# Kernel optimization log

Hardware: AMD Instinct MI355X
Metric: run time of the kernel (lower is better)

The kernel has to match this reference:

```python
import jax, jax.numpy as jnp
import numpy as np

B, LQ, LKV = 4, 512, 8192
Q_DIM, KV_DIM = 1024, 512
QK_CH, V_CH, N_HEADS = 256, 256, 8
EPS = 1e-5


def _layernorm(x, g, b):
    m = jnp.mean(x, axis=-1, keepdims=True)
    v = jnp.mean(jnp.square(x - m), axis=-1, keepdims=True)
    return (x - m) * jax.lax.rsqrt(v + EPS) * g + b


def setup_inputs() -> dict:
    key = jax.random.key(0)
    ks = jax.random.split(key, 8)
    hidden_states = jax.random.normal(ks[0], (B, LQ, Q_DIM), dtype=jnp.float32)
    inputs = jax.random.normal(ks[1], (B, LKV, KV_DIM), dtype=jnp.float32)
    # Linear weights stored as [in, out] for x @ W
    Wq = jax.random.normal(ks[2], (Q_DIM, QK_CH), dtype=jnp.float32) * (1.0 / np.sqrt(Q_DIM))
    Wk = jax.random.normal(ks[3], (KV_DIM, QK_CH), dtype=jnp.float32) * (1.0 / np.sqrt(KV_DIM))
    Wv = jax.random.normal(ks[4], (KV_DIM, V_CH), dtype=jnp.float32) * (1.0 / np.sqrt(KV_DIM))
    bq = jnp.zeros((QK_CH,), jnp.float32)
    bk = jax.random.normal(ks[5], (QK_CH,), dtype=jnp.float32) * 0.02
    bv = jax.random.normal(ks[6], (V_CH,), dtype=jnp.float32) * 0.02
    ln1_g = jnp.ones((Q_DIM,), jnp.float32)
    ln1_b = jnp.zeros((Q_DIM,), jnp.float32)
    ln2_g = jnp.ones((KV_DIM,), jnp.float32)
    ln2_b = jnp.zeros((KV_DIM,), jnp.float32)
    return dict(hidden_states=hidden_states, inputs=inputs,
                ln1_g=ln1_g, ln1_b=ln1_b, ln2_g=ln2_g, ln2_b=ln2_b,
                Wq=Wq, bq=bq, Wk=Wk, bk=bk, Wv=Wv, bv=bv)


def reference(hidden_states, inputs, ln1_g, ln1_b, ln2_g, ln2_b,
              Wq, bq, Wk, bk, Wv, bv):
    H = N_HEADS
    dqk = QK_CH // H
    dv = V_CH // H
    hs = _layernorm(hidden_states, ln1_g, ln1_b)          # [B,LQ,Q_DIM]
    inp = _layernorm(inputs, ln2_g, ln2_b)                # [B,LKV,KV_DIM]
    q = (hs @ Wq + bq).reshape(B, LQ, H, dqk)             # [B,LQ,H,dqk]
    k = (inp @ Wk + bk).reshape(B, LKV, H, dqk)           # [B,LKV,H,dqk]
    v = (inp @ Wv + bv).reshape(B, LKV, H, dv)            # [B,LKV,H,dv]
    scores = jnp.einsum('bqhd,bkhd->bhqk', q, k) / np.sqrt(dqk).astype(np.float32)
    probs = jax.nn.softmax(scores, axis=-1)               # [B,H,LQ,LKV] (materialized, as in torch)
    ctx = jnp.einsum('bhqk,bkhd->bqhd', probs, v)         # [B,LQ,H,dv]
    return ctx.reshape(B, LQ, H * dv)
```

## Files before the change

kernel.cpp:

```cpp
#include <hip/hip_runtime.h>
#include <hip/hip_bf16.h>
#include <math.h>

#define NB    4
#define LQ    512
#define LKV   8192
#define QDIM  1024
#define KVDIM 512
#define NH    8
#define EPS_LN 1e-5f
#define SMAX  12.0f

typedef __attribute__((ext_vector_type(8))) short bf16x8;
typedef __attribute__((ext_vector_type(4))) float f32x4;

static __device__ __forceinline__ ushort f2bf(float x) {
    unsigned int u = __builtin_bit_cast(unsigned int, x);
    u += 0x7FFFu + ((u >> 16) & 1u);
    return (ushort)(u >> 16);
}

#if __has_builtin(__builtin_amdgcn_cvt_pk_bf16_f32)
static __device__ __forceinline__ unsigned int pk_bf16(float a, float b) {
    auto r = __builtin_amdgcn_cvt_pk_bf16_f32(a, b);
    return __builtin_bit_cast(unsigned int, r);
}
#else
static __device__ __forceinline__ unsigned int pk_bf16(float a, float b) {
    return (unsigned int)f2bf(a) | ((unsigned int)f2bf(b) << 16);
}
#endif

#if __has_builtin(__builtin_amdgcn_exp2f)
#define EXP2F(x) __builtin_amdgcn_exp2f(x)
#else
#define EXP2F(x) exp2f(x)
#endif

static __device__ __forceinline__ void gld_lds16(const ushort* g, ushort* l) {
    __builtin_amdgcn_global_load_lds(
        (const __attribute__((address_space(1))) unsigned int*)g,
        (__attribute__((address_space(3))) unsigned int*)l, 16, 0, 0);
}

template<int K>
static __device__ __forceinline__ void ln_norm_row(
    const float* __restrict__ x, const float* __restrict__ g,
    const float* __restrict__ bta, ushort* __restrict__ y, int row, int lane)
{
    const float* xp = x + (size_t)row * K;
    constexpr int NV = K / 256;
    float4 v[NV];
    float s = 0.f;
#pragma unroll
    for (int i = 0; i < NV; ++i) {
        v[i] = *(const float4*)(xp + lane * 4 + i * 256);
        s += v[i].x + v[i].y + v[i].z + v[i].w;
    }
#pragma unroll
    for (int o = 1; o < 64; o <<= 1) s += __shfl_xor(s, o, 64);
    const float mu = s * (1.0f / K);
    float vs = 0.f;
#pragma unroll
    for (int i = 0; i < NV; ++i) {
        float dx = v[i].x - mu, dy = v[i].y - mu, dz = v[i].z - mu, dw = v[i].w - mu;
        vs += dx * dx + dy * dy + dz * dz + dw * dw;
    }
#pragma unroll
    for (int o = 1; o < 64; o <<= 1) vs += __shfl_xor(vs, o, 64);
    const float rs = rsqrtf(vs * (1.0f / K) + EPS_LN);
#pragma unroll
    for (int i = 0; i < NV; ++i) {
        const float4 gv = *(const float4*)(g   + lane * 4 + i * 256);
        const float4 bv = *(const float4*)(bta + lane * 4 + i * 256);
        uint2 o;
        o.x = pk_bf16((v[i].x - mu) * rs * gv.x + bv.x, (v[i].y - mu) * rs * gv.y + bv.y);
        o.y = pk_bf16((v[i].z - mu) * rs * gv.z + bv.z, (v[i].w - mu) * rs * gv.w + bv.w);
        *(uint2*)(y + (size_t)row * K + lane * 4 + i * 256) = o;
    }
}

static __device__ __forceinline__ void ln_stats_row(
    const float* __restrict__ x, float* __restrict__ mean, float* __restrict__ rstd,
    int row, int lane)
{
    const float* xp = x + (size_t)row * QDIM;
    float4 v[4];
    float s = 0.f;
#pragma unroll
    for (int i = 0; i < 4; ++i) {
        v[i] = *(const float4*)(xp + lane * 4 + i * 256);
        s += v[i].x + v[i].y + v[i].z + v[i].w;
    }
#pragma unroll
    for (int o = 1; o < 64; o <<= 1) s += __shfl_xor(s, o, 64);
    const float mu = s * (1.0f / QDIM);
    float vs = 0.f;
#pragma unroll
    for (int i = 0; i < 4; ++i) {
        float dx = v[i].x - mu, dy = v[i].y - mu, dz = v[i].z - mu, dw = v[i].w - mu;
        vs += dx * dx + dy * dy + dz * dz + dw * dw;
    }
#pragma unroll
    for (int o = 1; o < 64; o <<= 1) vs += __shfl_xor(vs, o, 64);
    if (lane == 0) {
        mean[row] = mu;
        rstd[row] = rsqrtf(vs * (1.0f / QDIM) + EPS_LN);
    }
}

static __device__ __forceinline__ void wt_transpose_body(
    const float* __restrict__ src, ushort* __restrict__ dst, int K,
    int kx, int ny, int t, ushort (*Ts)[72])
{
    const int k0 = kx * 64, n0 = ny * 64;
    const int nl = t & 63;
#pragma unroll
    for (int p = 0; p < 16; ++p) {
        const int kl = p * 4 + (t >> 6);
        Ts[nl][kl] = f2bf(src[(size_t)(k0 + kl) * 256 + n0 + nl]);
    }
    __syncthreads();
    const int ck = (t & 7) * 8;
#pragma unroll
    for (int p = 0; p < 2; ++p) {
        const int rn = p * 32 + (t >> 3);
        *(bf16x8*)(dst + (size_t)(n0 + rn) * K + k0 + ck) = *(const bf16x8*)&Ts[rn][ck];
    }
}

__global__ __launch_bounds__(256) void phaseA_kernel(
    const float* __restrict__ inputs, const float* __restrict__ ln2g,
    const float* __restrict__ ln2b,   ushort* __restrict__ Abf,
    const float* __restrict__ hidden, float* __restrict__ mean_h, float* __restrict__ rstd_h,
    const float* __restrict__ Wq, const float* __restrict__ Wk, const float* __restrict__ Wv,
    ushort* __restrict__ WtQ, ushort* __restrict__ WtKV)
{
    __shared__ ushort Ts[64][72];
    const int bid = blockIdx.x;
    const int t = threadIdx.x;
    const int lane = t & 63;
    if (bid < 8192) {
        ln_norm_row<KVDIM>(inputs, ln2g, ln2b, Abf, bid * 4 + (t >> 6), lane);
    } else if (bid < 8704) {
        ln_stats_row(hidden, mean_h, rstd_h, (bid - 8192) * 4 + (t >> 6), lane);
    } else if (bid < 8768) {
        const int p = bid - 8704;
        wt_transpose_body(Wq, WtQ, QDIM, p & 15, p >> 4, t, Ts);
    } else if (bid < 8800) {
        const int p = bid - 8768;
        wt_transpose_body(Wk, WtKV, KVDIM, p & 7, p >> 3, t, Ts);
    } else {
        const int p = bid - 8800;
        wt_transpose_body(Wv, WtKV + (size_t)256 * KVDIM, KVDIM, p & 7, p >> 3, t, Ts);
    }
}

__global__ __launch_bounds__(256) void phaseB_kernel(
    const ushort* __restrict__ Abf, const ushort* __restrict__ WtKV,
    const float* __restrict__ bk, const float* __restrict__ bv,
    ushort* __restrict__ kb, ushort* __restrict__ vt,
    const float* __restrict__ hidden, const float* __restrict__ mean_h,
    const float* __restrict__ rstd_h,
    const float* __restrict__ ln1g, const float* __restrict__ ln1b,
    const ushort* __restrict__ WtQ, const float* __restrict__ bq,
    ushort* __restrict__ qb, float oscale)
{
    __shared__ __align__(16) ushort SMEM[4 * 64 * 72];
    const int bid  = blockIdx.x;
    const int t    = threadIdx.x;
    const int lane = t & 63;
    const int w    = t >> 6;
    const int lq   = lane & 15;
    const int lg   = lane >> 4;
    const int wm   = w >> 1;
    const int wn   = w & 1;

    if (bid < 1024) {
        const int bm = (bid >> 2) * 128;
        const int bn = (bid & 3) * 128;
        ushort* As = SMEM;
        ushort* Bs = SMEM + 4096;

        const int srow = t >> 2;
        const int scol = ((t & 3) ^ ((t >> 3) & 3)) * 8;
        const ushort* gA = Abf  + (size_t)(bm + srow) * KVDIM + scol;
        const ushort* gB = WtKV + (size_t)(bn + srow) * KVDIM + scol;
        ushort* lA = As + t * 8;
        ushort* lB = Bs + t * 8;

        f32x4 acc[4][4] = {};
        for (int k0 = 0; k0 < KVDIM; k0 += 32) {
            gld_lds16(gA + k0,                       lA);
            gld_lds16(gA + (size_t)64 * KVDIM + k0,  lA + 2048);
            gld_lds16(gB + k0,                       lB);
            gld_lds16(gB + (size_t)64 * KVDIM + k0,  lB + 2048);
            __syncthreads();
            bf16x8 af[4], bf[4];
#pragma unroll
            for (int mt = 0; mt < 4; ++mt) {
                const int m = wm * 64 + mt * 16 + lq;
                af[mt] = *(const bf16x8*)(As + m * 32 + ((lg ^ ((m >> 1) & 3)) << 3));
            }
#pragma unroll
            for (int nt = 0; nt < 4; ++nt) {
                const int n = wn * 64 + nt * 16 + lq;
                bf[nt] = *(const bf16x8*)(Bs + n * 32 + ((lg ^ ((n >> 1) & 3)) << 3));
            }
#pragma unroll
            for (int mt = 0; mt < 4; ++mt)
#pragma unroll
                for (int nt = 0; nt < 4; ++nt)
                    acc[mt][nt] = __builtin_amdgcn_mfma_f32_16x16x32_bf16(af[mt], bf[nt], acc[mt][nt], 0, 0, 0);
            __syncthreads();
        }
        const int m0base = bm + wm * 64;
        const int bidx   = m0base >> 13;
        const int tokb   = m0base & 8191;

        if (bn < 256) {
            ushort (*Cs)[72] = (ushort(*)[72])(SMEM + w * 64 * 72);
#pragma unroll
            for (int nt = 0; nt < 4; ++nt) {
                const int n_l = nt * 16 + lq;
                const float bias = bk[bn + wn * 64 + n_l];
#pragma unroll
                for (int mt = 0; mt < 4; ++mt)
#pragma unroll
                    for (int r = 0; r < 4; ++r)
                        Cs[mt * 16 + lg * 4 + r][n_l] = f2bf(acc[mt][nt][r] + bias);
            }
            const int r0 = lane >> 3;
            const int ck = (lane & 7) * 8;
            const int nc = bn + wn * 64 + ck;
            const int h = nc >> 5, d = nc & 31;
            const size_t obase = (((size_t)(bidx * NH + h) << 13) + tokb) * 32 + d;
#pragma unroll
            for (int p = 0; p < 8; ++p) {
                const int row = p * 8 + r0;
                *(bf16x8*)(kb + obase + (size_t)row * 32) = *(const bf16x8*)&Cs[row][ck];
            }
        } else {
            ushort (*Cs)[72] = (ushort(*)[72])(SMEM + w * 64 * 72);
#pragma unroll
            for (int nt = 0; nt < 4; ++nt) {
                const int n_l = nt * 16 + lq;
                const float bias = bv[(bn - 256) + wn * 64 + n_l];
#pragma unroll
                for (int mt = 0; mt < 4; ++mt) {
                    uint2 o;
                    o.x = pk_bf16(acc[mt][nt][0] + bias, acc[mt][nt][1] + bias);
                    o.y = pk_bf16(acc[mt][nt][2] + bias, acc[mt][nt][3] + bias);
                    *(uint2*)&Cs[n_l][mt * 16 + lg * 4] = o;
                }
            }
            const int r0 = lane >> 3;
            const int cm = (lane & 7) * 8;
            const int tokc = tokb + cm;
#pragma unroll
            for (int p = 0; p < 8; ++p) {
                const int row = p * 8 + r0;
                const int nv  = (bn - 256) + wn * 64 + row;
                const int h = nv >> 5, d = nv & 31;
                *(bf16x8*)(vt + ((size_t)(bidx * NH + h) * 32 + d) * LKV + tokc) =
                    *(const bf16x8*)&Cs[row][cm];
            }
        }
    } else {
        const int p  = bid - 1024;
        const int bm = (p >> 2) * 64;
        const int bn = (p & 3) * 64;
        ushort* As = SMEM;
        ushort* Bs = SMEM + 4096;

        const int srow = t >> 3;
        const int scol = ((t & 7) ^ (srow & 7)) * 8;
        const ushort* gB = WtQ + (size_t)(bn + srow) * QDIM + scol;
        ushort* lB  = Bs + t * 8;
        ushort* lA0 = As + t * 8;
        ushort* lA1 = As + 2048 + t * 8;

        const int r0 = bm + srow;
        const float mu0 = mean_h[r0],      rs0 = rstd_h[r0];
        const float mu1 = mean_h[r0 + 32], rs1 = rstd_h[r0 + 32];
        const float* xA0 = hidden + (size_t)r0 * QDIM + scol;
        const float* xA1 = xA0 + (size_t)32 * QDIM;

        f32x4 acc[2][2] = {};
        for (int k0 = 0; k0 < QDIM; k0 += 64) {
            gld_lds16(gB + k0,                      lB);
            gld_lds16(gB + (size_t)32 * QDIM + k0,  lB + 2048);
            const float4 a0 = *(const float4*)(xA0 + k0);
            const float4 a1 = *(const float4*)(xA0 + k0 + 4);
            const float4 c0 = *(const float4*)(xA1 + k0);
            const float4 c1 = *(const float4*)(xA1 + k0 + 4);
            const float4 g0 = *(const float4*)(ln1g + k0 + scol);
            const float4 g1 = *(const float4*)(ln1g + k0 + scol + 4);
            const float4 d0 = *(const float4*)(ln1b + k0 + scol);
            const float4 d1 = *(const float4*)(ln1b + k0 + scol + 4);
            uint4 w0, w1;
            w0.x = pk_bf16((a0.x - mu0) * rs0 * g0.x + d0.x, (a0.y - mu0) * rs0 * g0.y + d0.y);
            w0.y = pk_bf16((a0.z - mu0) * rs0 * g0.z + d0.z, (a0.w - mu0) * rs0 * g0.w + d0.w);
            w0.z = pk_bf16((a1.x - mu0) * rs0 * g1.x + d1.x, (a1.y - mu0) * rs0 * g1.y + d1.y);
            w0.w = pk_bf16((a1.z - mu0) * rs0 * g1.z + d1.z, (a1.w - mu0) * rs0 * g1.w + d1.w);
            w1.x = pk_bf16((c0.x - mu1) * rs1 * g0.x + d0.x, (c0.y - mu1) * rs1 * g0.y + d0.y);
            w1.y = pk_bf16((c0.z - mu1) * rs1 * g0.z + d0.z, (c0.w - mu1) * rs1 * g0.w + d0.w);
            w1.z = pk_bf16((c1.x - mu1) * rs1 * g1.x + d1.x, (c1.y - mu1) * rs1 * g1.y + d1.y);
            w1.w = pk_bf16((c1.z - mu1) * rs1 * g1.z + d1.z, (c1.w - mu1) * rs1 * g1.w + d1.w);
            *(uint4*)lA0 = w0;
            *(uint4*)lA1 = w1;
            __syncthreads();
#pragma unroll
            for (int kh = 0; kh < 2; ++kh) {
                bf16x8 af[2], bf[2];
#pragma unroll
                for (int mt = 0; mt < 2; ++mt) {
                    const int m = wm * 32 + mt * 16 + lq;
                    af[mt] = *(const bf16x8*)(As + m * 64 + (((lg + 4 * kh) ^ (m & 7)) << 3));
                }
#pragma unroll
                for (int nt = 0; nt < 2; ++nt) {
                    const int n = wn * 32 + nt * 16 + lq;
                    bf[nt] = *(const bf16x8*)(Bs + n * 64 + (((lg + 4 * kh) ^ (n & 7)) << 3));
                }
#pragma unroll
                for (int mt = 0; mt < 2; ++mt)
#pragma unroll
                    for (int nt = 0; nt < 2; ++nt)
                        acc[mt][nt] = __builtin_amdgcn_mfma_f32_16x16x32_bf16(af[mt], bf[nt], acc[mt][nt], 0, 0, 0);
            }
            __syncthreads();
        }

#pragma unroll
        for (int nt = 0; nt < 2; ++nt) {
            const int n = bn + wn * 32 + nt * 16 + lq;
            const int h = n >> 5, d = n & 31;
            const float bias = bq[n];
#pragma unroll
            for (int mt = 0; mt < 2; ++mt) {
                const int m0   = bm + wm * 32 + mt * 16 + lg * 4;
                const int bidx = m0 >> 9;
                const int tok  = m0 & 511;
                const size_t base = (((size_t)(bidx * NH + h) << 9) + tok) * 32 + d;
#pragma unroll
                for (int r = 0; r < 4; ++r)
                    qb[base + (size_t)r * 32] = f2bf((acc[mt][nt][r] + bias) * oscale);
            }
        }
    }
}

__global__ __launch_bounds__(512, 4) void attn_mfma_kernel(
    const ushort* __restrict__ Qb,
    const ushort* __restrict__ Kb,
    const ushort* __restrict__ Vt,
    float* __restrict__ Out)
{
    const int bid = blockIdx.x;
    const int xcd = bid & 7;
    const int rr  = bid >> 3;
    const int bh  = ((rr & 3) << 3) | xcd;
    const int qt  = rr >> 2;
    const int b = bh >> 3, h = bh & 7;
    const int t = threadIdx.x, w = t >> 6, lane = t & 63;
    const int lq = lane & 15, lg = lane >> 4;

    __shared__ __align__(16) ushort Pb[2][8][32][72];
    __shared__ float lbuf[8][32];

    bf16x8 qfrag[2];
    const size_t qbase = ((size_t)bh * LQ + qt * 32) * 32;
    qfrag[0] = *(const bf16x8*)(Qb + qbase + (size_t)lq * 32 + lg * 8);
    qfrag[1] = *(const bf16x8*)(Qb + qbase + (size_t)(16 + lq) * 32 + lg * 8);

    const ushort* KpA = Kb + ((size_t)bh * LKV + w * 1024 + lq) * 32 + lg * 8;
    const ushort* VpA = Vt + ((size_t)bh * 32 + lq) * LKV + w * 1024 + lg * 8;

    f32x4 oacc[2][2] = {};
    float l_part[2] = {0.f, 0.f};
    const f32x4 cM = {-SMAX, -SMAX, -SMAX, -SMAX};

    bf16x8 kf[4], vf[2][2];
#pragma unroll
    for (int m = 0; m < 4; ++m)
        kf[m] = *(const bf16x8*)(KpA + (size_t)(m * 16) * 32);
#pragma unroll
    for (int dt = 0; dt < 2; ++dt)
#pragma unroll
        for (int hf = 0; hf < 2; ++hf)
            vf[dt][hf] = *(const bf16x8*)(VpA + (size_t)(dt * 16) * LKV + hf * 32);

    for (int kt = 0; kt < 1024; kt += 64) {
        bf16x8 kc[4], vc[2][2];
#pragma unroll
        for (int m = 0; m < 4; ++m) kc[m] = kf[m];
#pragma unroll
        for (int dt = 0; dt < 2; ++dt)
#pragma unroll
            for (int hf = 0; hf < 2; ++hf) vc[dt][hf] = vf[dt][hf];

        const int nk = (kt + 64 < 1024) ? kt + 64 : 0;
#pragma unroll
        for (int m = 0; m < 4; ++m)
            kf[m] = *(const bf16x8*)(KpA + (size_t)(nk + m * 16) * 32);
#pragma unroll
        for (int dt = 0; dt < 2; ++dt)
#pragma unroll
            for (int hf = 0; hf < 2; ++hf)
                vf[dt][hf] = *(const bf16x8*)(VpA + (size_t)(dt * 16) * LKV + nk + hf * 32);

        f32x4 s[4][2];
#pragma unroll
        for (int m = 0; m < 4; ++m)
#pragma unroll
            for (int n = 0; n < 2; ++n)
                s[m][n] = __builtin_amdgcn_mfma_f32_16x16x32_bf16(kc[m], qfrag[n], cM, 0, 0, 0);

        ushort* myP = &Pb[(kt >> 6) & 1][w][0][0];

#pragma unroll
        for (int n = 0; n < 2; ++n) {
#pragma unroll
            for (int m = 0; m < 4; ++m) {
                const float p0 = EXP2F(s[m][n][0]);
                const float p1 = EXP2F(s[m][n][1]);
                const float p2 = EXP2F(s[m][n][2]);
                const float p3 = EXP2F(s[m][n][3]);
                l_part[n] += ((p0 + p1) + (p2 + p3));
                uint2 pw;
                pw.x = pk_bf16(p0, p1);
                pw.y = pk_bf16(p2, p3);
                *(uint2*)(myP + (n * 16 + lq) * 72 + m * 16 + lg * 4) = pw;
            }
        }

        bf16x8 pf[2][2];
#pragma unroll
        for (int n = 0; n < 2; ++n)
#pragma unroll
            for (int hf = 0; hf < 2; ++hf)
                pf[n][hf] = *(const bf16x8*)(myP + (size_t)(n * 16 + lq) * 72 + hf * 32 + lg * 8);

#pragma unroll
        for (int dt = 0; dt < 2; ++dt)
#pragma unroll
            for (int n = 0; n < 2; ++n) {
                oacc[dt][n] = __builtin_amdgcn_mfma_f32_16x16x32_bf16(vc[dt][0], pf[n][0], oacc[dt][n], 0, 0, 0);
                oacc[dt][n] = __builtin_amdgcn_mfma_f32_16x16x32_bf16(vc[dt][1], pf[n][1], oacc[dt][n], 0, 0, 0);
            }
    }

#pragma unroll
    for (int n = 0; n < 2; ++n) {
        l_part[n] += __shfl_xor(l_part[n], 16);
        l_part[n] += __shfl_xor(l_part[n], 32);
    }
    if (lg == 0) {
        lbuf[w][lq]      = l_part[0];
        lbuf[w][16 + lq] = l_part[1];
    }
    __syncthreads();

    float* Ob = (float*)&Pb[0][0][0][0];
    if (w >= 4) {
#pragma unroll
        for (int n = 0; n < 2; ++n)
#pragma unroll
            for (int dt = 0; dt < 2; ++dt)
                *(f32x4*)&Ob[((size_t)(w - 4) * 32 + n * 16 + lq) * 36 + dt * 16 + lg * 4] = oacc[dt][n];
    }
    __syncthreads();
    if (w < 4) {
#pragma unroll
        for (int n = 0; n < 2; ++n)
#pragma unroll
            for (int dt = 0; dt < 2; ++dt) {
                float* p = &Ob[((size_t)w * 32 + n * 16 + lq) * 36 + dt * 16 + lg * 4];
                f32x4 v = *(f32x4*)p;
                v += oacc[dt][n];
                *(f32x4*)p = v;
            }
    }
    __syncthreads();
    {
        const int q  = t >> 4;
        const int d0 = (t & 15) * 2;
        float s0 = 0.f, s1 = 0.f;
#pragma unroll
        for (int j = 0; j < 4; ++j) {
            s0 += Ob[((size_t)j * 32 + q) * 36 + d0];
            s1 += Ob[((size_t)j * 32 + q) * 36 + d0 + 1];
        }
        float gl = 0.f;
#pragma unroll
        for (int j = 0; j < 8; ++j) gl += lbuf[j][q];
        const float inv = 1.0f / gl;
        float2 o; o.x = s0 * inv; o.y = s1 * inv;
        *(float2*)(Out + ((size_t)b * LQ + qt * 32 + q) * 256 + h * 32 + d0) = o;
    }
}

extern "C" void kernel_launch(void* const* d_in, const int* in_sizes, int n_in,
                              void* d_out, int out_size, void* d_ws, size_t ws_size,
                              hipStream_t stream)
{
    const float* hidden = (const float*)d_in[0];
    const float* inputs = (const float*)d_in[1];
    const float* ln1g   = (const float*)d_in[2];
    const float* ln1b   = (const float*)d_in[3];
    const float* ln2g   = (const float*)d_in[4];
    const float* ln2b   = (const float*)d_in[5];
    const float* Wq     = (const float*)d_in[6];
    const float* bq     = (const float*)d_in[7];
    const float* Wk     = (const float*)d_in[8];
    const float* bk     = (const float*)d_in[9];
    const float* Wv     = (const float*)d_in[10];
    const float* bv     = (const float*)d_in[11];
    float* out = (float*)d_out;

    char* wsb = (char*)d_ws;
    ushort* qb     = (ushort*)(wsb);
    ushort* WtKV   = (ushort*)(wsb + (1u << 20));
    ushort* WtQ    = (ushort*)(wsb + (1u << 20) + (512u << 10));
    float*  mean_h = (float*)(wsb + (2u << 20));
    float*  rstd_h = (float*)(wsb + (2u << 20) + 8192);
    ushort* kb     = (ushort*)(wsb + (2u << 20) + 16384);
    ushort* vt     = (ushort*)(wsb + (18u << 20) + 16384);
    ushort* Abf    = (ushort*)(wsb + (34u << 20) + 16384);

    const float oscale = 0.2550540226496112f;

    phaseA_kernel<<<8832, 256, 0, stream>>>(inputs, ln2g, ln2b, Abf,
                                            hidden, mean_h, rstd_h,
                                            Wq, Wk, Wv, WtQ, WtKV);
    phaseB_kernel<<<1152, 256, 0, stream>>>(Abf, WtKV, bk, bv, kb, vt,
                                            hidden, mean_h, rstd_h, ln1g, ln1b,
                                            WtQ, bq, qb, oscale);
    attn_mfma_kernel<<<512, 512, 0, stream>>>(qb, kb, vt, out);
}
```

Measured before the change: 215.1 us.

## Fuse KV layernorm into projection GEMM, retile Q GEMM, software-pipeline attention loop

Phase A now computes only per-row mean and rstd for the KV inputs, using single-pass sum and sum-of-squares. The normalized bf16 copy of the inputs is no longer written; the KV projection GEMM normalizes fp32 inputs on the fly with a register prefetch of the next k-slice and an XCD-aware block remap. The Q GEMM uses smaller tiles (more blocks) with prefetched LN inputs. The attention inner loop is restructured into 32-key steps with a double-buffered P tile, overlapping the PV MFMAs of the previous step with the QK and exp of the current one. Single-pass variance is less numerically robust, and the KV GEMM now reads fp32 activations, four times per row (once per N tile).

```diff
diff --git a/kernel.cpp b/kernel.cpp
--- a/kernel.cpp
+++ b/kernel.cpp
@@ -43,72 +43,6 @@
         (__attribute__((address_space(3))) unsigned int*)l, 16, 0, 0);
 }
 
-template<int K>
-static __device__ __forceinline__ void ln_norm_row(
-    const float* __restrict__ x, const float* __restrict__ g,
-    const float* __restrict__ bta, ushort* __restrict__ y, int row, int lane)
-{
-    const float* xp = x + (size_t)row * K;
-    constexpr int NV = K / 256;
-    float4 v[NV];
-    float s = 0.f;
-#pragma unroll
-    for (int i = 0; i < NV; ++i) {
-        v[i] = *(const float4*)(xp + lane * 4 + i * 256);
-        s += v[i].x + v[i].y + v[i].z + v[i].w;
-    }
-#pragma unroll
-    for (int o = 1; o < 64; o <<= 1) s += __shfl_xor(s, o, 64);
-    const float mu = s * (1.0f / K);
-    float vs = 0.f;
-#pragma unroll
-    for (int i = 0; i < NV; ++i) {
-        float dx = v[i].x - mu, dy = v[i].y - mu, dz = v[i].z - mu, dw = v[i].w - mu;
-        vs += dx * dx + dy * dy + dz * dz + dw * dw;
-    }
-#pragma unroll
-    for (int o = 1; o < 64; o <<= 1) vs += __shfl_xor(vs, o, 64);
-    const float rs = rsqrtf(vs * (1.0f / K) + EPS_LN);
-#pragma unroll
-    for (int i = 0; i < NV; ++i) {
-        const float4 gv = *(const float4*)(g   + lane * 4 + i * 256);
-        const float4 bv = *(const float4*)(bta + lane * 4 + i * 256);
-        uint2 o;
-        o.x = pk_bf16((v[i].x - mu) * rs * gv.x + bv.x, (v[i].y - mu) * rs * gv.y + bv.y);
-        o.y = pk_bf16((v[i].z - mu) * rs * gv.z + bv.z, (v[i].w - mu) * rs * gv.w + bv.w);
-        *(uint2*)(y + (size_t)row * K + lane * 4 + i * 256) = o;
-    }
-}
-
-static __device__ __forceinline__ void ln_stats_row(
-    const float* __restrict__ x, float* __restrict__ mean, float* __restrict__ rstd,
-    int row, int lane)
-{
-    const float* xp = x + (size_t)row * QDIM;
-    float4 v[4];
-    float s = 0.f;
-#pragma unroll
-    for (int i = 0; i < 4; ++i) {
-        v[i] = *(const float4*)(xp + lane * 4 + i * 256);
-        s += v[i].x + v[i].y + v[i].z + v[i].w;
-    }
-#pragma unroll
-    for (int o = 1; o < 64; o <<= 1) s += __shfl_xor(s, o, 64);
-    const float mu = s * (1.0f / QDIM);
-    float vs = 0.f;
-#pragma unroll
-    for (int i = 0; i < 4; ++i) {
-        float dx = v[i].x - mu, dy = v[i].y - mu, dz = v[i].z - mu, dw = v[i].w - mu;
-        vs += dx * dx + dy * dy + dz * dz + dw * dw;
-    }
-#pragma unroll
-    for (int o = 1; o < 64; o <<= 1) vs += __shfl_xor(vs, o, 64);
-    if (lane == 0) {
-        mean[row] = mu;
-        rstd[row] = rsqrtf(vs * (1.0f / QDIM) + EPS_LN);
-    }
-}
-
 static __device__ __forceinline__ void wt_transpose_body(
     const float* __restrict__ src, ushort* __restrict__ dst, int K,
     int kx, int ny, int t, ushort (*Ts)[72])
@@ -130,8 +64,7 @@
 }
 
 __global__ __launch_bounds__(256) void phaseA_kernel(
-    const float* __restrict__ inputs, const float* __restrict__ ln2g,
-    const float* __restrict__ ln2b,   ushort* __restrict__ Abf,
+    const float* __restrict__ inputs, float* __restrict__ mean_i, float* __restrict__ rstd_i,
     const float* __restrict__ hidden, float* __restrict__ mean_h, float* __restrict__ rstd_h,
     const float* __restrict__ Wq, const float* __restrict__ Wk, const float* __restrict__ Wv,
     ushort* __restrict__ WtQ, ushort* __restrict__ WtKV)
@@ -141,9 +74,39 @@
     const int t = threadIdx.x;
     const int lane = t & 63;
     if (bid < 8192) {
-        ln_norm_row<KVDIM>(inputs, ln2g, ln2b, Abf, bid * 4 + (t >> 6), lane);
+        const int row = bid * 4 + (t >> 6);
+        const float* xp = inputs + (size_t)row * KVDIM;
+        float s = 0.f, ss = 0.f;
+#pragma unroll
+        for (int i = 0; i < 2; ++i) {
+            const float4 v = *(const float4*)(xp + lane * 4 + i * 256);
+            s  += (v.x + v.y) + (v.z + v.w);
+            ss += (v.x * v.x + v.y * v.y) + (v.z * v.z + v.w * v.w);
+        }
+#pragma unroll
+        for (int o = 1; o < 64; o <<= 1) { s += __shfl_xor(s, o, 64); ss += __shfl_xor(ss, o, 64); }
+        if (lane == 0) {
+            const float mu = s * (1.0f / KVDIM);
+            mean_i[row] = mu;
+            rstd_i[row] = rsqrtf(ss * (1.0f / KVDIM) - mu * mu + EPS_LN);
+        }
     } else if (bid < 8704) {
-        ln_stats_row(hidden, mean_h, rstd_h, (bid - 8192) * 4 + (t >> 6), lane);
+        const int row = (bid - 8192) * 4 + (t >> 6);
+        const float* xp = hidden + (size_t)row * QDIM;
+        float s = 0.f, ss = 0.f;
+#pragma unroll
+        for (int i = 0; i < 4; ++i) {
+            const float4 v = *(const float4*)(xp + lane * 4 + i * 256);
+            s  += (v.x + v.y) + (v.z + v.w);
+            ss += (v.x * v.x + v.y * v.y) + (v.z * v.z + v.w * v.w);
+        }
+#pragma unroll
+        for (int o = 1; o < 64; o <<= 1) { s += __shfl_xor(s, o, 64); ss += __shfl_xor(ss, o, 64); }
+        if (lane == 0) {
+            const float mu = s * (1.0f / QDIM);
+            mean_h[row] = mu;
+            rstd_h[row] = rsqrtf(ss * (1.0f / QDIM) - mu * mu + EPS_LN);
+        }
     } else if (bid < 8768) {
         const int p = bid - 8704;
         wt_transpose_body(Wq, WtQ, QDIM, p & 15, p >> 4, t, Ts);
@@ -157,11 +120,14 @@
 }
 
 __global__ __launch_bounds__(256) void phaseB_kernel(
-    const ushort* __restrict__ Abf, const ushort* __restrict__ WtKV,
+    const float* __restrict__ inputs,
+    const float* __restrict__ mean_i, const float* __restrict__ rstd_i,
+    const float* __restrict__ ln2g, const float* __restrict__ ln2b,
+    const ushort* __restrict__ WtKV,
     const float* __restrict__ bk, const float* __restrict__ bv,
     ushort* __restrict__ kb, ushort* __restrict__ vt,
-    const float* __restrict__ hidden, const float* __restrict__ mean_h,
-    const float* __restrict__ rstd_h,
+    const float* __restrict__ hidden,
+    const float* __restrict__ mean_h, const float* __restrict__ rstd_h,
     const float* __restrict__ ln1g, const float* __restrict__ ln1b,
     const ushort* __restrict__ WtQ, const float* __restrict__ bq,
     ushort* __restrict__ qb, float oscale)
@@ -177,24 +143,59 @@
     const int wn   = w & 1;
 
     if (bid < 1024) {
-        const int bm = (bid >> 2) * 128;
-        const int bn = (bid & 3) * 128;
+        const int x  = bid & 7;
+        const int j  = bid >> 3;
+        const int bm = (x * 32 + (j >> 2)) * 128;
+        const int bn = (j & 3) * 128;
         ushort* As = SMEM;
         ushort* Bs = SMEM + 4096;
 
         const int srow = t >> 2;
         const int scol = ((t & 3) ^ ((t >> 3) & 3)) * 8;
-        const ushort* gA = Abf  + (size_t)(bm + srow) * KVDIM + scol;
         const ushort* gB = WtKV + (size_t)(bn + srow) * KVDIM + scol;
-        ushort* lA = As + t * 8;
-        ushort* lB = Bs + t * 8;
+        ushort* lB  = Bs + t * 8;
+        ushort* lA0 = As + t * 8;
+        ushort* lA1 = As + 2048 + t * 8;
+
+        const int r0 = bm + srow;
+        const float rs0 = rstd_i[r0],      mr0 = -mean_i[r0] * rs0;
+        const float rs1 = rstd_i[r0 + 64], mr1 = -mean_i[r0 + 64] * rs1;
+        const float* xp0 = inputs + (size_t)r0 * KVDIM + scol;
+        const float* xp1 = xp0 + (size_t)64 * KVDIM;
+
+        float4 a0 = *(const float4*)(xp0);
+        float4 a1 = *(const float4*)(xp0 + 4);
+        float4 c0 = *(const float4*)(xp1);
+        float4 c1 = *(const float4*)(xp1 + 4);
+        float4 g0 = *(const float4*)(ln2g + scol);
+        float4 g1 = *(const float4*)(ln2g + scol + 4);
+        float4 e0 = *(const float4*)(ln2b + scol);
+        float4 e1 = *(const float4*)(ln2b + scol + 4);
 
         f32x4 acc[4][4] = {};
         for (int k0 = 0; k0 < KVDIM; k0 += 32) {
-            gld_lds16(gA + k0,                       lA);
-            gld_lds16(gA + (size_t)64 * KVDIM + k0,  lA + 2048);
             gld_lds16(gB + k0,                       lB);
             gld_lds16(gB + (size_t)64 * KVDIM + k0,  lB + 2048);
+            uint4 w0, w1;
+            w0.x = pk_bf16(fmaf(fmaf(a0.x, rs0, mr0), g0.x, e0.x), fmaf(fmaf(a0.y, rs0, mr0), g0.y, e0.y));
+            w0.y = pk_bf16(fmaf(fmaf(a0.z, rs0, mr0), g0.z, e0.z), fmaf(fmaf(a0.w, rs0, mr0), g0.w, e0.w));
+            w0.z = pk_bf16(fmaf(fmaf(a1.x, rs0, mr0), g1.x, e1.x), fmaf(fmaf(a1.y, rs0, mr0), g1.y, e1.y));
+            w0.w = pk_bf16(fmaf(fmaf(a1.z, rs0, mr0), g1.z, e1.z), fmaf(fmaf(a1.w, rs0, mr0), g1.w, e1.w));
+            w1.x = pk_bf16(fmaf(fmaf(c0.x, rs1, mr1), g0.x, e0.x), fmaf(fmaf(c0.y, rs1, mr1), g0.y, e0.y));
+            w1.y = pk_bf16(fmaf(fmaf(c0.z, rs1, mr1), g0.z, e0.z), fmaf(fmaf(c0.w, rs1, mr1), g0.w, e0.w));
+            w1.z = pk_bf16(fmaf(fmaf(c1.x, rs1, mr1), g1.x, e1.x), fmaf(fmaf(c1.y, rs1, mr1), g1.y, e1.y));
+            w1.w = pk_bf16(fmaf(fmaf(c1.z, rs1, mr1), g1.z, e1.z), fmaf(fmaf(c1.w, rs1, mr1), g1.w, e1.w));
+            *(uint4*)lA0 = w0;
+            *(uint4*)lA1 = w1;
+            const int nk = (k0 + 32 < KVDIM) ? k0 + 32 : 0;
+            a0 = *(const float4*)(xp0 + nk);
+            a1 = *(const float4*)(xp0 + nk + 4);
+            c0 = *(const float4*)(xp1 + nk);
+            c1 = *(const float4*)(xp1 + nk + 4);
+            g0 = *(const float4*)(ln2g + nk + scol);
+            g1 = *(const float4*)(ln2g + nk + scol + 4);
+            e0 = *(const float4*)(ln2b + nk + scol);
+            e1 = *(const float4*)(ln2b + nk + scol + 4);
             __syncthreads();
             bf16x8 af[4], bf[4];
 #pragma unroll
@@ -214,6 +215,7 @@
                     acc[mt][nt] = __builtin_amdgcn_mfma_f32_16x16x32_bf16(af[mt], bf[nt], acc[mt][nt], 0, 0, 0);
             __syncthreads();
         }
+
         const int m0base = bm + wm * 64;
         const int bidx   = m0base >> 13;
         const int tokb   = m0base & 8191;
@@ -230,14 +232,14 @@
                     for (int r = 0; r < 4; ++r)
                         Cs[mt * 16 + lg * 4 + r][n_l] = f2bf(acc[mt][nt][r] + bias);
             }
-            const int r0 = lane >> 3;
-            const int ck = (lane & 7) * 8;
-            const int nc = bn + wn * 64 + ck;
+            const int r0_ = lane >> 3;
+            const int ck  = (lane & 7) * 8;
+            const int nc  = bn + wn * 64 + ck;
             const int h = nc >> 5, d = nc & 31;
             const size_t obase = (((size_t)(bidx * NH + h) << 13) + tokb) * 32 + d;
 #pragma unroll
             for (int p = 0; p < 8; ++p) {
-                const int row = p * 8 + r0;
+                const int row = p * 8 + r0_;
                 *(bf16x8*)(kb + obase + (size_t)row * 32) = *(const bf16x8*)&Cs[row][ck];
             }
         } else {
@@ -254,12 +256,12 @@
                     *(uint2*)&Cs[n_l][mt * 16 + lg * 4] = o;
                 }
             }
-            const int r0 = lane >> 3;
-            const int cm = (lane & 7) * 8;
+            const int r0_ = lane >> 3;
+            const int cm  = (lane & 7) * 8;
             const int tokc = tokb + cm;
 #pragma unroll
             for (int p = 0; p < 8; ++p) {
-                const int row = p * 8 + r0;
+                const int row = p * 8 + r0_;
                 const int nv  = (bn - 256) + wn * 64 + row;
                 const int h = nv >> 5, d = nv & 31;
                 *(bf16x8*)(vt + ((size_t)(bidx * NH + h) * 32 + d) * LKV + tokc) =
@@ -268,66 +270,58 @@
         }
     } else {
         const int p  = bid - 1024;
-        const int bm = (p >> 2) * 64;
-        const int bn = (p & 3) * 64;
+        const int x  = p & 7;
+        const int j  = p >> 3;
+        const int bm = (x * 8 + (j >> 2)) * 32;
+        const int bn = (j & 3) * 64;
         ushort* As = SMEM;
-        ushort* Bs = SMEM + 4096;
+        ushort* Bs = SMEM + 2048;
 
         const int srow = t >> 3;
         const int scol = ((t & 7) ^ (srow & 7)) * 8;
         const ushort* gB = WtQ + (size_t)(bn + srow) * QDIM + scol;
-        ushort* lB  = Bs + t * 8;
-        ushort* lA0 = As + t * 8;
-        ushort* lA1 = As + 2048 + t * 8;
-
-        const int r0 = bm + srow;
-        const float mu0 = mean_h[r0],      rs0 = rstd_h[r0];
-        const float mu1 = mean_h[r0 + 32], rs1 = rstd_h[r0 + 32];
-        const float* xA0 = hidden + (size_t)r0 * QDIM + scol;
-        const float* xA1 = xA0 + (size_t)32 * QDIM;
-
-        f32x4 acc[2][2] = {};
+        ushort* lB = Bs + t * 8;
+        ushort* lA = As + t * 8;
+
+        const int r = bm + srow;
+        const float rs0 = rstd_h[r], mr0 = -mean_h[r] * rs0;
+        const float* xA = hidden + (size_t)r * QDIM + scol;
+
+        float4 a0 = *(const float4*)(xA);
+        float4 a1 = *(const float4*)(xA + 4);
+        float4 g0 = *(const float4*)(ln1g + scol);
+        float4 g1 = *(const float4*)(ln1g + scol + 4);
+        float4 e0 = *(const float4*)(ln1b + scol);
+        float4 e1 = *(const float4*)(ln1b + scol + 4);
+
+        f32x4 acc[2] = {};
         for (int k0 = 0; k0 < QDIM; k0 += 64) {
             gld_lds16(gB + k0,                      lB);
             gld_lds16(gB + (size_t)32 * QDIM + k0,  lB + 2048);
-            const float4 a0 = *(const float4*)(xA0 + k0);
-            const float4 a1 = *(const float4*)(xA0 + k0 + 4);
-            const float4 c0 = *(const float4*)(xA1 + k0);
-            const float4 c1 = *(const float4*)(xA1 + k0 + 4);
-            const float4 g0 = *(const float4*)(ln1g + k0 + scol);
-            const float4 g1 = *(const float4*)(ln1g + k0 + scol + 4);
-            const float4 d0 = *(const float4*)(ln1b + k0 + scol);
-            const float4 d1 = *(const float4*)(ln1b + k0 + scol + 4);
-            uint4 w0, w1;
-            w0.x = pk_bf16((a0.x - mu0) * rs0 * g0.x + d0.x, (a0.y - mu0) * rs0 * g0.y + d0.y);
-            w0.y = pk_bf16((a0.z - mu0) * rs0 * g0.z + d0.z, (a0.w - mu0) * rs0 * g0.w + d0.w);
-            w0.z = pk_bf16((a1.x - mu0) * rs0 * g1.x + d1.x, (a1.y - mu0) * rs0 * g1.y + d1.y);
-            w0.w = pk_bf16((a1.z - mu0) * rs0 * g1.z + d1.z, (a1.w - mu0) * rs0 * g1.w + d1.w);
-            w1.x = pk_bf16((c0.x - mu1) * rs1 * g0.x + d0.x, (c0.y - mu1) * rs1 * g0.y + d0.y);
-            w1.y = pk_bf16((c0.z - mu1) * rs1 * g0.z + d0.z, (c0.w - mu1) * rs1 * g0.w + d0.w);
-            w1.z = pk_bf16((c1.x - mu1) * rs1 * g1.x + d1.x, (c1.y - mu1) * rs1 * g1.y + d1.y);
-            w1.w = pk_bf16((c1.z - mu1) * rs1 * g1.z + d1.z, (c1.w - mu1) * rs1 * g1.w + d1.w);
-            *(uint4*)lA0 = w0;
-            *(uint4*)lA1 = w1;
+            uint4 w0;
+            w0.x = pk_bf16(fmaf(fmaf(a0.x, rs0, mr0), g0.x, e0.x), fmaf(fmaf(a0.y, rs0, mr0), g0.y, e0.y));
+            w0.y = pk_bf16(fmaf(fmaf(a0.z, rs0, mr0), g0.z, e0.z), fmaf(fmaf(a0.w, rs0, mr0), g0.w, e0.w));
+            w0.z = pk_bf16(fmaf(fmaf(a1.x, rs0, mr0), g1.x, e1.x), fmaf(fmaf(a1.y, rs0, mr0), g1.y, e1.y));
+            w0.w = pk_bf16(fmaf(fmaf(a1.z, rs0, mr0), g1.z, e1.z), fmaf(fmaf(a1.w, rs0, mr0), g1.w, e1.w));
+            *(uint4*)lA = w0;
+            const int nk = (k0 + 64 < QDIM) ? k0 + 64 : 0;
+            a0 = *(const float4*)(xA + nk);
+            a1 = *(const float4*)(xA + nk + 4);
+            g0 = *(const float4*)(ln1g + nk + scol);
+            g1 = *(const float4*)(ln1g + nk + scol + 4);
+            e0 = *(const float4*)(ln1b + nk + scol);
+            e1 = *(const float4*)(ln1b + nk + scol + 4);
             __syncthreads();
 #pragma unroll
             for (int kh = 0; kh < 2; ++kh) {
-                bf16x8 af[2], bf[2];
-#pragma unroll
-                for (int mt = 0; mt < 2; ++mt) {
-                    const int m = wm * 32 + mt * 16 + lq;
-                    af[mt] = *(const bf16x8*)(As + m * 64 + (((lg + 4 * kh) ^ (m & 7)) << 3));
-                }
+                const int m = wm * 16 + lq;
+                const bf16x8 af = *(const bf16x8*)(As + m * 64 + (((lg + 4 * kh) ^ (m & 7)) << 3));
 #pragma unroll
                 for (int nt = 0; nt < 2; ++nt) {
                     const int n = wn * 32 + nt * 16 + lq;
-                    bf[nt] = *(const bf16x8*)(Bs + n * 64 + (((lg + 4 * kh) ^ (n & 7)) << 3));
+                    const bf16x8 bf = *(const bf16x8*)(Bs + n * 64 + (((lg + 4 * kh) ^ (n & 7)) << 3));
+                    acc[nt] = __builtin_amdgcn_mfma_f32_16x16x32_bf16(af, bf, acc[nt], 0, 0, 0);
                 }
-#pragma unroll
-                for (int mt = 0; mt < 2; ++mt)
-#pragma unroll
-                    for (int nt = 0; nt < 2; ++nt)
-                        acc[mt][nt] = __builtin_amdgcn_mfma_f32_16x16x32_bf16(af[mt], bf[nt], acc[mt][nt], 0, 0, 0);
             }
             __syncthreads();
         }
@@ -337,16 +331,13 @@
             const int n = bn + wn * 32 + nt * 16 + lq;
             const int h = n >> 5, d = n & 31;
             const float bias = bq[n];
-#pragma unroll
-            for (int mt = 0; mt < 2; ++mt) {
-                const int m0   = bm + wm * 32 + mt * 16 + lg * 4;
-                const int bidx = m0 >> 9;
-                const int tok  = m0 & 511;
-                const size_t base = (((size_t)(bidx * NH + h) << 9) + tok) * 32 + d;
-#pragma unroll
-                for (int r = 0; r < 4; ++r)
-                    qb[base + (size_t)r * 32] = f2bf((acc[mt][nt][r] + bias) * oscale);
-            }
+            const int m0   = bm + wm * 16 + lg * 4;
+            const int bidx = m0 >> 9;
+            const int tok  = m0 & 511;
+            const size_t base = (((size_t)(bidx * NH + h) << 9) + tok) * 32 + d;
+#pragma unroll
+            for (int rr_ = 0; rr_ < 4; ++rr_)
+                qb[base + (size_t)rr_ * 32] = f2bf((acc[nt][rr_] + bias) * oscale);
         }
     }
 }
@@ -366,7 +357,7 @@
     const int t = threadIdx.x, w = t >> 6, lane = t & 63;
     const int lq = lane & 15, lg = lane >> 4;
 
-    __shared__ __align__(16) ushort Pb[2][8][32][72];
+    __shared__ __align__(16) ushort Pb[2][8][32][40];
     __shared__ float lbuf[8][32];
 
     bf16x8 qfrag[2];
@@ -381,75 +372,86 @@
     float l_part[2] = {0.f, 0.f};
     const f32x4 cM = {-SMAX, -SMAX, -SMAX, -SMAX};
 
-    bf16x8 kf[4], vf[2][2];
-#pragma unroll
-    for (int m = 0; m < 4; ++m)
-        kf[m] = *(const bf16x8*)(KpA + (size_t)(m * 16) * 32);
-#pragma unroll
-    for (int dt = 0; dt < 2; ++dt)
-#pragma unroll
-        for (int hf = 0; hf < 2; ++hf)
-            vf[dt][hf] = *(const bf16x8*)(VpA + (size_t)(dt * 16) * LKV + hf * 32);
-
-    for (int kt = 0; kt < 1024; kt += 64) {
-        bf16x8 kc[4], vc[2][2];
-#pragma unroll
-        for (int m = 0; m < 4; ++m) kc[m] = kf[m];
-#pragma unroll
-        for (int dt = 0; dt < 2; ++dt)
-#pragma unroll
-            for (int hf = 0; hf < 2; ++hf) vc[dt][hf] = vf[dt][hf];
-
-        const int nk = (kt + 64 < 1024) ? kt + 64 : 0;
-#pragma unroll
-        for (int m = 0; m < 4; ++m)
-            kf[m] = *(const bf16x8*)(KpA + (size_t)(nk + m * 16) * 32);
-#pragma unroll
-        for (int dt = 0; dt < 2; ++dt)
-#pragma unroll
-            for (int hf = 0; hf < 2; ++hf)
-                vf[dt][hf] = *(const bf16x8*)(VpA + (size_t)(dt * 16) * LKV + nk + hf * 32);
-
-        f32x4 s[4][2];
-#pragma unroll
-        for (int m = 0; m < 4; ++m)
-#pragma unroll
-            for (int n = 0; n < 2; ++n)
-                s[m][n] = __builtin_amdgcn_mfma_f32_16x16x32_bf16(kc[m], qfrag[n], cM, 0, 0, 0);
-
-        ushort* myP = &Pb[(kt >> 6) & 1][w][0][0];
-
-#pragma unroll
-        for (int n = 0; n < 2; ++n) {
-#pragma unroll
-            for (int m = 0; m < 4; ++m) {
-                const float p0 = EXP2F(s[m][n][0]);
-                const float p1 = EXP2F(s[m][n][1]);
-                const float p2 = EXP2F(s[m][n][2]);
-                const float p3 = EXP2F(s[m][n][3]);
-                l_part[n] += ((p0 + p1) + (p2 + p3));
-                uint2 pw;
-                pw.x = pk_bf16(p0, p1);
-                pw.y = pk_bf16(p2, p3);
-                *(uint2*)(myP + (n * 16 + lq) * 72 + m * 16 + lg * 4) = pw;
-            }
-        }
-
-        bf16x8 pf[2][2];
-#pragma unroll
-        for (int n = 0; n < 2; ++n)
-#pragma unroll
-            for (int hf = 0; hf < 2; ++hf)
-                pf[n][hf] = *(const bf16x8*)(myP + (size_t)(n * 16 + lq) * 72 + hf * 32 + lg * 8);
-
-#pragma unroll
-        for (int dt = 0; dt < 2; ++dt)
-#pragma unroll
-            for (int n = 0; n < 2; ++n) {
-                oacc[dt][n] = __builtin_amdgcn_mfma_f32_16x16x32_bf16(vc[dt][0], pf[n][0], oacc[dt][n], 0, 0, 0);
-                oacc[dt][n] = __builtin_amdgcn_mfma_f32_16x16x32_bf16(vc[dt][1], pf[n][1], oacc[dt][n], 0, 0, 0);
-            }
-    }
+    ushort* P0 = &Pb[0][w][0][0];
+    ushort* P1 = &Pb[1][w][0][0];
+
+    bf16x8 kf0 = *(const bf16x8*)(KpA);
+    bf16x8 kf1 = *(const bf16x8*)(KpA + 16 * 32);
+    bf16x8 vf0 = *(const bf16x8*)(VpA);
+    bf16x8 vf1 = *(const bf16x8*)(VpA + (size_t)16 * LKV);
+
+    bf16x8 vp0, vp1;
+
+#define ATTN_EXPW(Pdst, s00, s10, s01, s11)                                              \
+    do {                                                                                 \
+        float p0, p1, p2, p3; uint2 pw;                                                  \
+        p0 = EXP2F((s00)[0]); p1 = EXP2F((s00)[1]); p2 = EXP2F((s00)[2]); p3 = EXP2F((s00)[3]); \
+        l_part[0] += (p0 + p1) + (p2 + p3);                                              \
+        pw.x = pk_bf16(p0, p1); pw.y = pk_bf16(p2, p3);                                  \
+        *(uint2*)((Pdst) + (lq) * 40 + lg * 4) = pw;                                     \
+        p0 = EXP2F((s10)[0]); p1 = EXP2F((s10)[1]); p2 = EXP2F((s10)[2]); p3 = EXP2F((s10)[3]); \
+        l_part[0] += (p0 + p1) + (p2 + p3);                                              \
+        pw.x = pk_bf16(p0, p1); pw.y = pk_bf16(p2, p3);                                  \
+        *(uint2*)((Pdst) + (lq) * 40 + 16 + lg * 4) = pw;                                \
+        p0 = EXP2F((s01)[0]); p1 = EXP2F((s01)[1]); p2 = EXP2F((s01)[2]); p3 = EXP2F((s01)[3]); \
+        l_part[1] += (p0 + p1) + (p2 + p3);                                              \
+        pw.x = pk_bf16(p0, p1); pw.y = pk_bf16(p2, p3);                                  \
+        *(uint2*)((Pdst) + (16 + lq) * 40 + lg * 4) = pw;                                \
+        p0 = EXP2F((s11)[0]); p1 = EXP2F((s11)[1]); p2 = EXP2F((s11)[2]); p3 = EXP2F((s11)[3]); \
+        l_part[1] += (p0 + p1) + (p2 + p3);                                              \
+        pw.x = pk_bf16(p0, p1); pw.y = pk_bf16(p2, p3);                                  \
+        *(uint2*)((Pdst) + (16 + lq) * 40 + 16 + lg * 4) = pw;                           \
+    } while (0)
+
+    {
+        const bf16x8 kc0 = kf0, kc1 = kf1;
+        vp0 = vf0; vp1 = vf1;
+        kf0 = *(const bf16x8*)(KpA + (size_t)32 * 32);
+        kf1 = *(const bf16x8*)(KpA + (size_t)48 * 32);
+        vf0 = *(const bf16x8*)(VpA + 32);
+        vf1 = *(const bf16x8*)(VpA + (size_t)16 * LKV + 32);
+        f32x4 s00 = __builtin_amdgcn_mfma_f32_16x16x32_bf16(kc0, qfrag[0], cM, 0, 0, 0);
+        f32x4 s01 = __builtin_amdgcn_mfma_f32_16x16x32_bf16(kc0, qfrag[1], cM, 0, 0, 0);
+        f32x4 s10 = __builtin_amdgcn_mfma_f32_16x16x32_bf16(kc1, qfrag[0], cM, 0, 0, 0);
+        f32x4 s11 = __builtin_amdgcn_mfma_f32_16x16x32_bf16(kc1, qfrag[1], cM, 0, 0, 0);
+        ATTN_EXPW(P0, s00, s10, s01, s11);
+    }
+
+    for (int kt = 32; kt < 1024; kt += 32) {
+        ushort* Pw = (kt & 32) ? P1 : P0;
+        ushort* Pr = (kt & 32) ? P0 : P1;
+        const bf16x8 kc0 = kf0, kc1 = kf1, vc0 = vf0, vc1 = vf1;
+        const int nk = (kt + 32 < 1024) ? kt + 32 : 0;
+        kf0 = *(const bf16x8*)(KpA + (size_t)nk * 32);
+        kf1 = *(const bf16x8*)(KpA + (size_t)(nk + 16) * 32);
+        vf0 = *(const bf16x8*)(VpA + nk);
+        vf1 = *(const bf16x8*)(VpA + (size_t)16 * LKV + nk);
+
+        f32x4 s00 = __builtin_amdgcn_mfma_f32_16x16x32_bf16(kc0, qfrag[0], cM, 0, 0, 0);
+        f32x4 s01 = __builtin_amdgcn_mfma_f32_16x16x32_bf16(kc0, qfrag[1], cM, 0, 0, 0);
+        f32x4 s10 = __builtin_amdgcn_mfma_f32_16x16x32_bf16(kc1, qfrag[0], cM, 0, 0, 0);
+        f32x4 s11 = __builtin_amdgcn_mfma_f32_16x16x32_bf16(kc1, qfrag[1], cM, 0, 0, 0);
+
+        const bf16x8 pf0 = *(const bf16x8*)(Pr + (size_t)lq * 40 + lg * 8);
+        const bf16x8 pf1 = *(const bf16x8*)(Pr + (size_t)(16 + lq) * 40 + lg * 8);
+        oacc[0][0] = __builtin_amdgcn_mfma_f32_16x16x32_bf16(vp0, pf0, oacc[0][0], 0, 0, 0);
+        oacc[0][1] = __builtin_amdgcn_mfma_f32_16x16x32_bf16(vp0, pf1, oacc[0][1], 0, 0, 0);
+        oacc[1][0] = __builtin_amdgcn_mfma_f32_16x16x32_bf16(vp1, pf0, oacc[1][0], 0, 0, 0);
+        oacc[1][1] = __builtin_amdgcn_mfma_f32_16x16x32_bf16(vp1, pf1, oacc[1][1], 0, 0, 0);
+        vp0 = vc0; vp1 = vc1;
+
+        ATTN_EXPW(Pw, s00, s10, s01, s11);
+    }
+
+    {
+        const bf16x8 pf0 = *(const bf16x8*)(P1 + (size_t)lq * 40 + lg * 8);
+        const bf16x8 pf1 = *(const bf16x8*)(P1 + (size_t)(16 + lq) * 40 + lg * 8);
+        oacc[0][0] = __builtin_amdgcn_mfma_f32_16x16x32_bf16(vp0, pf0, oacc[0][0], 0, 0, 0);
+        oacc[0][1] = __builtin_amdgcn_mfma_f32_16x16x32_bf16(vp0, pf1, oacc[0][1], 0, 0, 0);
+        oacc[1][0] = __builtin_amdgcn_mfma_f32_16x16x32_bf16(vp1, pf0, oacc[1][0], 0, 0, 0);
+        oacc[1][1] = __builtin_amdgcn_mfma_f32_16x16x32_bf16(vp1, pf1, oacc[1][1], 0, 0, 0);
+    }
+#undef ATTN_EXPW
 
 #pragma unroll
     for (int n = 0; n < 2; ++n) {
@@ -523,18 +525,20 @@
     ushort* qb     = (ushort*)(wsb);
     ushort* WtKV   = (ushort*)(wsb + (1u << 20));
     ushort* WtQ    = (ushort*)(wsb + (1u << 20) + (512u << 10));
-    float*  mean_h = (float*)(wsb + (2u << 20));
-    float*  rstd_h = (float*)(wsb + (2u << 20) + 8192);
-    ushort* kb     = (ushort*)(wsb + (2u << 20) + 16384);
-    ushort* vt     = (ushort*)(wsb + (18u << 20) + 16384);
-    ushort* Abf    = (ushort*)(wsb + (34u << 20) + 16384);
+    float*  mean_i = (float*)(wsb + (2u << 20));
+    float*  rstd_i = (float*)(wsb + (2u << 20) + (128u << 10));
+    float*  mean_h = (float*)(wsb + (2u << 20) + (256u << 10));
+    float*  rstd_h = (float*)(wsb + (2u << 20) + (264u << 10));
+    ushort* kb     = (ushort*)(wsb + (2u << 20) + (512u << 10));
+    ushort* vt     = (ushort*)(wsb + (18u << 20) + (512u << 10));
 
     const float oscale = 0.2550540226496112f;
 
-    phaseA_kernel<<<8832, 256, 0, stream>>>(inputs, ln2g, ln2b, Abf,
+    phaseA_kernel<<<8832, 256, 0, stream>>>(inputs, mean_i, rstd_i,
                                             hidden, mean_h, rstd_h,
                                             Wq, Wk, Wv, WtQ, WtKV);
-    phaseB_kernel<<<1152, 256, 0, stream>>>(Abf, WtKV, bk, bv, kb, vt,
+    phaseB_kernel<<<1280, 256, 0, stream>>>(inputs, mean_i, rstd_i, ln2g, ln2b,
+                                            WtKV, bk, bv, kb, vt,
                                             hidden, mean_h, rstd_h, ln1g, ln1b,
                                             WtQ, bq, qb, oscale);
     attn_mfma_kernel<<<512, 512, 0, stream>>>(qb, kb, vt, out);
```

New measurement: 218.9 us. Within noise of the previous version (+1.8%).
